# Optimization experiments

Measured on AMD Instinct MI355X. Metric: run time of the kernel, lower is better.

The kernel has to match this reference:

```python
import jax, jax.numpy as jnp
import numpy as np

B, S, H = 2, 2048, 1024
NUM_HEAD = 16
HEAD_HIDDEN = H // NUM_HEAD
SCALE = float(np.sqrt(HEAD_HIDDEN))  # 8.0
INF = 10000000000.0


def setup_inputs() -> dict:
    key = jax.random.key(0)
    ks = jax.random.split(key, 12)
    std = 1.0 / np.sqrt(H)
    mk = lambda k: (jax.random.normal(k, (H, H), jnp.float32) * std)
    return {
        "query": jax.random.normal(ks[0], (B, S, H), jnp.float32),
        "key": jax.random.normal(ks[1], (B, S, H), jnp.float32),
        "value": jax.random.normal(ks[2], (B, S, H), jnp.float32),
        "att_mask": jnp.ones((B, 1, 1, S), jnp.float32),
        "wq": mk(ks[3]), "bq": jnp.zeros((H,), jnp.float32),
        "wk": mk(ks[4]), "bk": jnp.zeros((H,), jnp.float32),
        "wv": mk(ks[5]), "bv": jnp.zeros((H,), jnp.float32),
        "wo": mk(ks[6]), "bo": jnp.zeros((H,), jnp.float32),
    }


def reference(query, key, value, att_mask, wq, bq, wk, bk, wv, bv, wo, bo):
    # projections (weights stored as [in, out])
    q = query @ wq + bq
    k = key @ wk + bk
    v = value @ wv + bv
    # split heads: [B, S, nH, hd]
    q = q.reshape(B, S, NUM_HEAD, HEAD_HIDDEN)
    k = k.reshape(B, S, NUM_HEAD, HEAD_HIDDEN)
    v = v.reshape(B, S, NUM_HEAD, HEAD_HIDDEN)
    # scores [B, nH, Sq, Sk], first divide by scale
    att = jnp.einsum("bqhd,bkhd->bhqk", q, k) / SCALE
    # additive mask applied BEFORE the second scale division (faithful quirk)
    att = att + (1.0 - att_mask) * (-INF)
    att = jax.nn.softmax(att / SCALE, axis=-1)
    out = jnp.einsum("bhqk,bkhd->bqhd", att, v).reshape(B, S, H)
    return out @ wo + bo
```

## Files before the change

### kernel.cpp

```cpp
#include <hip/hip_runtime.h>
#include <cstdint>

typedef unsigned short u16;
typedef __attribute__((ext_vector_type(8))) short bf16x8;
typedef __attribute__((ext_vector_type(4))) float f32x4;

#define S_LEN 2048
#define HDIM  1024
#define NHEAD 16

__device__ __forceinline__ float bf2f(u16 u){ return __uint_as_float(((uint32_t)u) << 16); }
__device__ __forceinline__ u16 f2bf(float f){
  uint32_t x = __float_as_uint(f);
  return (u16)((x + 0x7fffu + ((x >> 16) & 1u)) >> 16);
}

__device__ __forceinline__ void gload_lds16(const void* g, void* l){
  __builtin_amdgcn_global_load_lds((const __attribute__((address_space(1))) void*)g,
                                   (__attribute__((address_space(3))) void*)l, 16, 0, 0);
}

__global__ __launch_bounds__(256) void k_cvt3(const float* __restrict__ q, const float* __restrict__ k,
                                              const float* __restrict__ v, u16* __restrict__ oq,
                                              u16* __restrict__ ok, u16* __restrict__ ov){
  int z = blockIdx.y;
  const float* in = z == 0 ? q : (z == 1 ? k : v);
  u16* out = z == 0 ? oq : (z == 1 ? ok : ov);
  int i = blockIdx.x * 256 + threadIdx.x;
  float4 f0 = *(const float4*)&in[(size_t)i * 8];
  float4 f1 = *(const float4*)&in[(size_t)i * 8 + 4];
  bf16x8 o;
  o[0] = (short)f2bf(f0.x); o[1] = (short)f2bf(f0.y);
  o[2] = (short)f2bf(f0.z); o[3] = (short)f2bf(f0.w);
  o[4] = (short)f2bf(f1.x); o[5] = (short)f2bf(f1.y);
  o[6] = (short)f2bf(f1.z); o[7] = (short)f2bf(f1.w);
  *(bf16x8*)&out[(size_t)i * 8] = o;
}

__global__ __launch_bounds__(256) void k_tr_w4(const float* __restrict__ w0, const float* __restrict__ w1,
                                               const float* __restrict__ w2, const float* __restrict__ w3,
                                               u16* __restrict__ o0, u16* __restrict__ o1,
                                               u16* __restrict__ o2, u16* __restrict__ o3){
  int z = blockIdx.z;
  const float* in = z == 0 ? w0 : (z == 1 ? w1 : (z == 2 ? w2 : w3));
  u16* out = z == 0 ? o0 : (z == 1 ? o1 : (z == 2 ? o2 : o3));
  __shared__ float t[64][65];
  int r0 = threadIdx.x >> 6;
  int c  = threadIdx.x & 63;
  int bx = blockIdx.x * 64, by = blockIdx.y * 64;
  #pragma unroll
  for (int i = 0; i < 64; i += 4) t[r0 + i][c] = in[(size_t)(by + r0 + i) * 1024 + bx + c];
  __syncthreads();
  #pragma unroll
  for (int i = 0; i < 64; i += 4) out[(size_t)(bx + r0 + i) * 1024 + by + c] = f2bf(t[c][r0 + i]);
}

__global__ __launch_bounds__(256) void k_tr_v(const u16* __restrict__ v, u16* __restrict__ vt){
  __shared__ u16 t[64][65];
  int r0 = threadIdx.x >> 6, c = threadIdx.x & 63;
  int s0 = blockIdx.x * 64;
  int bh = blockIdx.y;
  int b = bh >> 4, h = bh & 15;
  const u16* src = v + (size_t)b * S_LEN * HDIM + h * 64;
  #pragma unroll
  for (int i = 0; i < 64; i += 4) t[r0 + i][c] = src[(size_t)(s0 + r0 + i) * HDIM + c];
  __syncthreads();
  u16* dst = vt + (size_t)bh * 64 * S_LEN + s0;
  #pragma unroll
  for (int i = 0; i < 64; i += 4) dst[(size_t)(r0 + i) * S_LEN + c] = t[c][r0 + i];
}

__global__ __launch_bounds__(256) void k_gemm_qkv(const u16* __restrict__ A0, const u16* __restrict__ A1,
                                                  const u16* __restrict__ A2,
                                                  const u16* __restrict__ W0, const u16* __restrict__ W1,
                                                  const u16* __restrict__ W2,
                                                  const float* __restrict__ b0, const float* __restrict__ b1,
                                                  const float* __restrict__ b2,
                                                  u16* __restrict__ C0, u16* __restrict__ C1,
                                                  u16* __restrict__ C2)
{
  int z = blockIdx.z;
  const u16* A  = z == 0 ? A0 : (z == 1 ? A1 : A2);
  const u16* Wt = z == 0 ? W0 : (z == 1 ? W1 : W2);
  const float* bias = z == 0 ? b0 : (z == 1 ? b1 : b2);
  u16* C = z == 0 ? C0 : (z == 1 ? C1 : C2);
  float scale = z == 0 ? (1.0f / 64.0f) : 1.0f;

  __shared__ u16 As[128 * 32];
  __shared__ u16 Bs[128 * 32];
  const int K = 1024, N = 1024;
  int tid = threadIdx.x;
  int lane = tid & 63, wave = tid >> 6;
  int quad = lane >> 4, c16 = lane & 15;
  int wm = wave >> 1, wn = wave & 1;
  int m0 = blockIdx.x * 128, n0 = blockIdx.y * 128;

  f32x4 acc[4][4] = {};

  for (int k0 = 0; k0 < K; k0 += 32) {
    #pragma unroll
    for (int i = 0; i < 2; i++) {
      int slot = tid + i * 256;
      int r = slot >> 2, cc = (slot & 3) * 8;
      gload_lds16(&A [(size_t)(m0 + r) * K + k0 + cc], &As[slot * 8]);
      gload_lds16(&Wt[(size_t)(n0 + r) * K + k0 + cc], &Bs[slot * 8]);
    }
    __syncthreads();
    bf16x8 af[4], bfr[4];
    #pragma unroll
    for (int mt = 0; mt < 4; mt++) af[mt]  = *(const bf16x8*)&As[(wm * 64 + mt * 16 + c16) * 32 + quad * 8];
    #pragma unroll
    for (int nt = 0; nt < 4; nt++) bfr[nt] = *(const bf16x8*)&Bs[(wn * 64 + nt * 16 + c16) * 32 + quad * 8];
    #pragma unroll
    for (int mt = 0; mt < 4; mt++)
      #pragma unroll
      for (int nt = 0; nt < 4; nt++)
        acc[mt][nt] = __builtin_amdgcn_mfma_f32_16x16x32_bf16(af[mt], bfr[nt], acc[mt][nt], 0, 0, 0);
    __syncthreads();
  }

  #pragma unroll
  for (int nt = 0; nt < 4; nt++) {
    int gc = n0 + wn * 64 + nt * 16 + c16;
    float bv = bias[gc];
    #pragma unroll
    for (int mt = 0; mt < 4; mt++)
      #pragma unroll
      for (int r = 0; r < 4; r++) {
        int gr = m0 + wm * 64 + mt * 16 + quad * 4 + r;
        C[(size_t)gr * N + gc] = f2bf((acc[mt][nt][r] + bv) * scale);
      }
  }
}

__global__ __launch_bounds__(256) void k_gemm_o(const u16* __restrict__ A, const u16* __restrict__ Wt,
                                                const float* __restrict__ bias, float* __restrict__ C)
{
  __shared__ u16 As[128 * 32];
  __shared__ u16 Bs[64 * 32];
  const int K = 1024, N = 1024;
  int tid = threadIdx.x;
  int lane = tid & 63, wave = tid >> 6;
  int quad = lane >> 4, c16 = lane & 15;
  int wm = wave >> 1, wn = wave & 1;
  int m0 = blockIdx.x * 128, n0 = blockIdx.y * 64;

  f32x4 acc[4][2] = {};

  for (int k0 = 0; k0 < K; k0 += 32) {
    #pragma unroll
    for (int i = 0; i < 2; i++) {
      int slot = tid + i * 256;
      int r = slot >> 2, cc = (slot & 3) * 8;
      gload_lds16(&A[(size_t)(m0 + r) * K + k0 + cc], &As[slot * 8]);
    }
    {
      int r = tid >> 2, cc = (tid & 3) * 8;
      gload_lds16(&Wt[(size_t)(n0 + r) * K + k0 + cc], &Bs[tid * 8]);
    }
    __syncthreads();
    bf16x8 af[4], bfr[2];
    #pragma unroll
    for (int mt = 0; mt < 4; mt++) af[mt]  = *(const bf16x8*)&As[(wm * 64 + mt * 16 + c16) * 32 + quad * 8];
    #pragma unroll
    for (int nt = 0; nt < 2; nt++) bfr[nt] = *(const bf16x8*)&Bs[(wn * 32 + nt * 16 + c16) * 32 + quad * 8];
    #pragma unroll
    for (int mt = 0; mt < 4; mt++)
      #pragma unroll
      for (int nt = 0; nt < 2; nt++)
        acc[mt][nt] = __builtin_amdgcn_mfma_f32_16x16x32_bf16(af[mt], bfr[nt], acc[mt][nt], 0, 0, 0);
    __syncthreads();
  }

  #pragma unroll
  for (int nt = 0; nt < 2; nt++) {
    int gc = n0 + wn * 32 + nt * 16 + c16;
    float bv = bias[gc];
    #pragma unroll
    for (int mt = 0; mt < 4; mt++)
      #pragma unroll
      for (int r = 0; r < 4; r++) {
        int gr = m0 + wm * 64 + mt * 16 + quad * 4 + r;
        C[(size_t)gr * N + gc] = acc[mt][nt][r] + bv;
      }
  }
}

__global__ __launch_bounds__(256, 2) void k_attn(const u16* __restrict__ Qm,
                                                 const u16* __restrict__ Km,
                                                 const u16* __restrict__ VTm,
                                                 const float* __restrict__ mask,
                                                 u16* __restrict__ Om)
{
  __shared__ u16 Ks[2][64 * 72];
  __shared__ u16 VTs[2][64 * 72];
  __shared__ u16 Ps[128][72];
  __shared__ float Msall[S_LEN];
  int tid = threadIdx.x;
  int lane = tid & 63, wave = tid >> 6;
  int quad = lane >> 4, c16 = lane & 15;
  int qb = blockIdx.x, h = blockIdx.y, b = blockIdx.z;
  const size_t SH = (size_t)S_LEN * HDIM;
  const u16* Qbase  = Qm + (size_t)b * SH + (size_t)qb * 128 * HDIM + h * 64;
  const u16* Kbase  = Km + (size_t)b * SH + h * 64;
  const u16* VTbase = VTm + (size_t)(b * NHEAD + h) * 64 * S_LEN;
  const float* Mbase = mask + (size_t)b * S_LEN;

  auto stage = [&](int s0, int bb) {
    #pragma unroll
    for (int i = 0; i < 5; i++) {
      int c = i * 256 + tid;
      if (c < 576) {
        int r = c / 9, cc = c - r * 9;
        int col = (cc == 8) ? 0 : cc * 8;
        gload_lds16(&Kbase[(size_t)(s0 + r) * HDIM + col], &Ks[bb][c * 8]);
      } else if (c < 1152) {
        int c2 = c - 576;
        int r = c2 / 9, cc = c2 - r * 9;
        int col = (cc == 8) ? 0 : cc * 8;
        gload_lds16(&VTbase[(size_t)r * S_LEN + s0 + col], &VTs[bb][c2 * 8]);
      }
    }
  };

  for (int i = tid; i < S_LEN; i += 256) Msall[i] = (1.0f - Mbase[i]) * (-1.25e9f);

  int qw0 = wave * 32;

  bf16x8 aq[2][2];
  #pragma unroll
  for (int mt = 0; mt < 2; mt++)
    #pragma unroll
    for (int kk = 0; kk < 2; kk++)
      aq[mt][kk] = *(const bf16x8*)&Qbase[(size_t)(qw0 + mt * 16 + c16) * HDIM + kk * 32 + quad * 8];

  f32x4 oacc[2][4] = {};
  float lsum[2][4] = {};

  stage(0, 0);
  __syncthreads();

  for (int kt = 0; kt < S_LEN / 64; kt++) {
    int s0 = kt * 64;
    int cb = kt & 1;
    if (kt + 1 < S_LEN / 64) stage(s0 + 64, cb ^ 1);

    f32x4 sacc[2][4] = {};
    #pragma unroll
    for (int kk = 0; kk < 2; kk++) {
      bf16x8 bk[4];
      #pragma unroll
      for (int nt = 0; nt < 4; nt++) bk[nt] = *(const bf16x8*)&Ks[cb][(nt * 16 + c16) * 72 + kk * 32 + quad * 8];
      #pragma unroll
      for (int mt = 0; mt < 2; mt++)
        #pragma unroll
        for (int nt = 0; nt < 4; nt++)
          sacc[mt][nt] = __builtin_amdgcn_mfma_f32_16x16x32_bf16(aq[mt][kk], bk[nt], sacc[mt][nt], 0, 0, 0);
    }

    #pragma unroll
    for (int nt = 0; nt < 4; nt++) {
      float madd = Msall[s0 + nt * 16 + c16];
      #pragma unroll
      for (int mt = 0; mt < 2; mt++)
        #pragma unroll
        for (int r = 0; r < 4; r++) {
          float p = __expf(sacc[mt][nt][r] + madd);
          lsum[mt][r] += p;
          Ps[qw0 + mt * 16 + quad * 4 + r][nt * 16 + c16] = f2bf(p);
        }
    }

    #pragma unroll
    for (int kk = 0; kk < 2; kk++) {
      bf16x8 pa[2], vb[4];
      #pragma unroll
      for (int mt = 0; mt < 2; mt++) pa[mt] = *(const bf16x8*)&Ps[qw0 + mt * 16 + c16][kk * 32 + quad * 8];
      #pragma unroll
      for (int nt = 0; nt < 4; nt++) vb[nt] = *(const bf16x8*)&VTs[cb][(nt * 16 + c16) * 72 + kk * 32 + quad * 8];
      #pragma unroll
      for (int mt = 0; mt < 2; mt++)
        #pragma unroll
        for (int nt = 0; nt < 4; nt++)
          oacc[mt][nt] = __builtin_amdgcn_mfma_f32_16x16x32_bf16(pa[mt], vb[kk == 0 ? nt : nt], oacc[mt][nt], 0, 0, 0);
    }
    __syncthreads();
  }

  #pragma unroll
  for (int mt = 0; mt < 2; mt++)
    #pragma unroll
    for (int r = 0; r < 4; r++) {
      float v = lsum[mt][r];
      v += __shfl_xor(v, 1); v += __shfl_xor(v, 2); v += __shfl_xor(v, 4); v += __shfl_xor(v, 8);
      lsum[mt][r] = v;
    }

  u16* Obase = Om + (size_t)b * SH + (size_t)qb * 128 * HDIM + h * 64;
  #pragma unroll
  for (int mt = 0; mt < 2; mt++)
    #pragma unroll
    for (int nt = 0; nt < 4; nt++)
      #pragma unroll
      for (int r = 0; r < 4; r++) {
        int lr = qw0 + mt * 16 + quad * 4 + r;
        Obase[(size_t)lr * HDIM + nt * 16 + c16] = f2bf(oacc[mt][nt][r] / lsum[mt][r]);
      }
}

extern "C" void kernel_launch(void* const* d_in, const int* in_sizes, int n_in,
                              void* d_out, int out_size, void* d_ws, size_t ws_size,
                              hipStream_t stream)
{
  (void)in_sizes; (void)n_in; (void)out_size; (void)ws_size;
  const float* q_in = (const float*)d_in[0];
  const float* k_in = (const float*)d_in[1];
  const float* v_in = (const float*)d_in[2];
  const float* mask = (const float*)d_in[3];
  const float* wq   = (const float*)d_in[4];
  const float* bq   = (const float*)d_in[5];
  const float* wk   = (const float*)d_in[6];
  const float* bk   = (const float*)d_in[7];
  const float* wv   = (const float*)d_in[8];
  const float* bv   = (const float*)d_in[9];
  const float* wo   = (const float*)d_in[10];
  const float* bo   = (const float*)d_in[11];

  u16* ws  = (u16*)d_ws;
  u16* wqt = ws;
  u16* wkt = wqt + (1u << 20);
  u16* wvt = wkt + (1u << 20);
  u16* wot = wvt + (1u << 20);
  u16* qi_ = wot + (1u << 20);
  u16* ki_ = qi_ + (4u << 20);
  u16* vi_ = ki_ + (4u << 20);
  u16* qb_ = vi_ + (4u << 20);
  u16* kb_ = qb_ + (4u << 20);
  u16* vb_ = kb_ + (4u << 20);
  u16* vtb = vb_ + (4u << 20);
  u16* ob_ = vtb + (4u << 20);

  dim3 blk(256);
  k_cvt3<<<dim3(2048, 3), blk, 0, stream>>>(q_in, k_in, v_in, qi_, ki_, vi_);
  k_tr_w4<<<dim3(16, 16, 4), blk, 0, stream>>>(wq, wk, wv, wo, wqt, wkt, wvt, wot);
  k_gemm_qkv<<<dim3(32, 8, 3), blk, 0, stream>>>(qi_, ki_, vi_, wqt, wkt, wvt, bq, bk, bv, qb_, kb_, vb_);
  k_tr_v<<<dim3(32, 32), blk, 0, stream>>>(vb_, vtb);
  k_attn<<<dim3(16, 16, 2), blk, 0, stream>>>(qb_, kb_, vtb, mask, ob_);
  k_gemm_o<<<dim3(32, 16), blk, 0, stream>>>(ob_, wot, bo, (float*)d_out);
}
```

Before: 239.9 us.

## Keep softmax probabilities in registers via transposed S^T MFMA, drop LDS P staging

The score product is now computed transposed (K as the A operand, Q as the B operand), so each lane's accumulator output already has the operand layout a 16x16x16 bf16 MFMA expects for P·V. The P buffer in shared memory and its write/read round trip are removed, and the mask is preloaded into the accumulator init. Row sums are reduced with fewer shuffles, and the output is normalized with a reciprocal multiply. The smaller 16x16x16 MFMA doubles the instruction count for the P·V product and relies on inline-asm packed bf16 conversion.

```diff
diff --git a/kernel.cpp b/kernel.cpp
--- a/kernel.cpp
+++ b/kernel.cpp
@@ -3,6 +3,7 @@
 
 typedef unsigned short u16;
 typedef __attribute__((ext_vector_type(8))) short bf16x8;
+typedef __attribute__((ext_vector_type(4))) short bf16x4;
 typedef __attribute__((ext_vector_type(4))) float f32x4;
 
 #define S_LEN 2048
@@ -194,7 +195,6 @@
 {
   __shared__ u16 Ks[2][64 * 72];
   __shared__ u16 VTs[2][64 * 72];
-  __shared__ u16 Ps[128][72];
   __shared__ float Msall[S_LEN];
   int tid = threadIdx.x;
   int lane = tid & 63, wave = tid >> 6;
@@ -227,15 +227,15 @@
 
   int qw0 = wave * 32;
 
-  bf16x8 aq[2][2];
-  #pragma unroll
-  for (int mt = 0; mt < 2; mt++)
+  bf16x8 bq[2][2];
+  #pragma unroll
+  for (int qt = 0; qt < 2; qt++)
     #pragma unroll
     for (int kk = 0; kk < 2; kk++)
-      aq[mt][kk] = *(const bf16x8*)&Qbase[(size_t)(qw0 + mt * 16 + c16) * HDIM + kk * 32 + quad * 8];
+      bq[qt][kk] = *(const bf16x8*)&Qbase[(size_t)(qw0 + qt * 16 + c16) * HDIM + kk * 32 + quad * 8];
 
   f32x4 oacc[2][4] = {};
-  float lsum[2][4] = {};
+  float lsq[2] = {};
 
   stage(0, 0);
   __syncthreads();
@@ -245,67 +245,80 @@
     int cb = kt & 1;
     if (kt + 1 < S_LEN / 64) stage(s0 + 64, cb ^ 1);
 
-    f32x4 sacc[2][4] = {};
+    f32x4 madd[4];
+    #pragma unroll
+    for (int kvt = 0; kvt < 4; kvt++) madd[kvt] = *(const f32x4*)&Msall[s0 + kvt * 16 + quad * 4];
+
+    f32x4 sacc[4][2];
+    #pragma unroll
+    for (int kvt = 0; kvt < 4; kvt++)
+      #pragma unroll
+      for (int qt = 0; qt < 2; qt++)
+        sacc[kvt][qt] = madd[kvt];
     #pragma unroll
     for (int kk = 0; kk < 2; kk++) {
-      bf16x8 bk[4];
-      #pragma unroll
-      for (int nt = 0; nt < 4; nt++) bk[nt] = *(const bf16x8*)&Ks[cb][(nt * 16 + c16) * 72 + kk * 32 + quad * 8];
-      #pragma unroll
-      for (int mt = 0; mt < 2; mt++)
+      bf16x8 ak[4];
+      #pragma unroll
+      for (int kvt = 0; kvt < 4; kvt++)
+        ak[kvt] = *(const bf16x8*)&Ks[cb][(kvt * 16 + c16) * 72 + kk * 32 + quad * 8];
+      #pragma unroll
+      for (int kvt = 0; kvt < 4; kvt++)
         #pragma unroll
-        for (int nt = 0; nt < 4; nt++)
-          sacc[mt][nt] = __builtin_amdgcn_mfma_f32_16x16x32_bf16(aq[mt][kk], bk[nt], sacc[mt][nt], 0, 0, 0);
-    }
-
-    #pragma unroll
-    for (int nt = 0; nt < 4; nt++) {
-      float madd = Msall[s0 + nt * 16 + c16];
-      #pragma unroll
-      for (int mt = 0; mt < 2; mt++)
+        for (int qt = 0; qt < 2; qt++)
+          sacc[kvt][qt] = __builtin_amdgcn_mfma_f32_16x16x32_bf16(ak[kvt], bq[qt][kk], sacc[kvt][qt], 0, 0, 0);
+    }
+
+    bf16x4 pa[2][4];
+    #pragma unroll
+    for (int kvt = 0; kvt < 4; kvt++)
+      #pragma unroll
+      for (int qt = 0; qt < 2; qt++) {
+        float p0 = __expf(sacc[kvt][qt][0]);
+        float p1 = __expf(sacc[kvt][qt][1]);
+        float p2 = __expf(sacc[kvt][qt][2]);
+        float p3 = __expf(sacc[kvt][qt][3]);
+        lsq[qt] += (p0 + p1) + (p2 + p3);
+        union { uint32_t u[2]; bf16x4 v; } cv;
+        asm("v_cvt_pk_bf16_f32 %0, %1, %2" : "=v"(cv.u[0]) : "v"(p0), "v"(p1));
+        asm("v_cvt_pk_bf16_f32 %0, %1, %2" : "=v"(cv.u[1]) : "v"(p2), "v"(p3));
+        pa[qt][kvt] = cv.v;
+      }
+
+    #pragma unroll
+    for (int kvt = 0; kvt < 4; kvt++) {
+      bf16x4 vb[4];
+      #pragma unroll
+      for (int dt = 0; dt < 4; dt++)
+        vb[dt] = *(const bf16x4*)&VTs[cb][(dt * 16 + c16) * 72 + kvt * 16 + quad * 4];
+      #pragma unroll
+      for (int qt = 0; qt < 2; qt++)
         #pragma unroll
-        for (int r = 0; r < 4; r++) {
-          float p = __expf(sacc[mt][nt][r] + madd);
-          lsum[mt][r] += p;
-          Ps[qw0 + mt * 16 + quad * 4 + r][nt * 16 + c16] = f2bf(p);
-        }
-    }
-
-    #pragma unroll
-    for (int kk = 0; kk < 2; kk++) {
-      bf16x8 pa[2], vb[4];
-      #pragma unroll
-      for (int mt = 0; mt < 2; mt++) pa[mt] = *(const bf16x8*)&Ps[qw0 + mt * 16 + c16][kk * 32 + quad * 8];
-      #pragma unroll
-      for (int nt = 0; nt < 4; nt++) vb[nt] = *(const bf16x8*)&VTs[cb][(nt * 16 + c16) * 72 + kk * 32 + quad * 8];
-      #pragma unroll
-      for (int mt = 0; mt < 2; mt++)
-        #pragma unroll
-        for (int nt = 0; nt < 4; nt++)
-          oacc[mt][nt] = __builtin_amdgcn_mfma_f32_16x16x32_bf16(pa[mt], vb[kk == 0 ? nt : nt], oacc[mt][nt], 0, 0, 0);
-    }
-    __syncthreads();
-  }
-
-  #pragma unroll
-  for (int mt = 0; mt < 2; mt++)
+        for (int dt = 0; dt < 4; dt++)
+          oacc[qt][dt] = __builtin_amdgcn_mfma_f32_16x16x16bf16_1k(pa[qt][kvt], vb[dt], oacc[qt][dt], 0, 0, 0);
+    }
+    __syncthreads();
+  }
+
+  #pragma unroll
+  for (int qt = 0; qt < 2; qt++) {
+    float v = lsq[qt];
+    v += __shfl_xor(v, 16);
+    v += __shfl_xor(v, 32);
+    lsq[qt] = v;
+  }
+
+  u16* Obase = Om + (size_t)b * SH + (size_t)qb * 128 * HDIM + h * 64;
+  #pragma unroll
+  for (int qt = 0; qt < 2; qt++)
     #pragma unroll
     for (int r = 0; r < 4; r++) {
-      float v = lsum[mt][r];
-      v += __shfl_xor(v, 1); v += __shfl_xor(v, 2); v += __shfl_xor(v, 4); v += __shfl_xor(v, 8);
-      lsum[mt][r] = v;
-    }
-
-  u16* Obase = Om + (size_t)b * SH + (size_t)qb * 128 * HDIM + h * 64;
-  #pragma unroll
-  for (int mt = 0; mt < 2; mt++)
-    #pragma unroll
-    for (int nt = 0; nt < 4; nt++)
-      #pragma unroll
-      for (int r = 0; r < 4; r++) {
-        int lr = qw0 + mt * 16 + quad * 4 + r;
-        Obase[(size_t)lr * HDIM + nt * 16 + c16] = f2bf(oacc[mt][nt][r] / lsum[mt][r]);
-      }
+      float l = __shfl(lsq[qt], quad * 4 + r);
+      float rinv = 1.0f / l;
+      int lr = qw0 + qt * 16 + quad * 4 + r;
+      #pragma unroll
+      for (int dt = 0; dt < 4; dt++)
+        Obase[(size_t)lr * HDIM + dt * 16 + c16] = f2bf(oacc[qt][dt][r] * rinv);
+    }
 }
 
 extern "C" void kernel_launch(void* const* d_in, const int* in_sizes, int n_in,
```

Result: faster. 227.1 us (-5.3%).
